# Performance work log

Hardware: AMD Instinct MI355X
Metric: run time of the kernel (lower is better)

## Reference

```python
import jax, jax.numpy as jnp
import numpy as np

B, H, S, D = 2, 16, 2048, 64
MASK_NEG = 1e9


def setup_inputs() -> dict:
    key = jax.random.key(0)
    kq, kk, kv, km = jax.random.split(key, 4)
    Q = jax.random.normal(kq, (B, H, S, D), dtype=jnp.float32)
    K = jax.random.normal(kk, (B, H, S, D), dtype=jnp.float32)
    V = jax.random.normal(kv, (B, H, S, D), dtype=jnp.float32)
    # float 0/1 mask, broadcast over heads; 1 = masked-out position
    attn_mask = jax.random.randint(km, (B, 1, S, S), 0, 2).astype(jnp.float32)
    return {"Q": Q, "K": K, "V": V, "attn_mask": attn_mask}


def reference(Q, K, V, attn_mask):
    # scores: [B, H, S, S]
    attn_score = jnp.einsum('bhqd,bhkd->bhqk', Q, K)
    scale = jnp.sqrt(jnp.asarray(K.shape[-1], dtype=jnp.float32))
    attn_scale = attn_score / scale - MASK_NEG * attn_mask
    attn_prob = jax.nn.softmax(attn_scale, axis=-1)
    attn_out = jnp.einsum('bhqk,bhkd->bhqd', attn_prob, V)
    return attn_out
```

## Files before the change

### kernel.cpp

```cpp
#include <hip/hip_runtime.h>


#define S_LEN 2048
#define D_DIM 64
#define WPR   32
#define NIT   32

typedef __attribute__((ext_vector_type(8)))  short bf16x8;
typedef __attribute__((ext_vector_type(4)))  float f32x4;
typedef __attribute__((ext_vector_type(16))) float f32x16;
typedef unsigned uint2v __attribute__((ext_vector_type(2)));
typedef unsigned long long ull;

__device__ __forceinline__ f32x16 mfma32(bf16x8 a, bf16x8 b, f32x16 c) {
  return __builtin_amdgcn_mfma_f32_32x32x16_bf16(a, b, c, 0, 0, 0);
}
__device__ __forceinline__ f32x4 mfma16(bf16x8 a, bf16x8 b, f32x4 c) {
  return __builtin_amdgcn_mfma_f32_16x16x32_bf16(a, b, c, 0, 0, 0);
}
__device__ __forceinline__ unsigned short f2bf(float f) {
  unsigned u = __builtin_bit_cast(unsigned, f);
  unsigned r = u + 0x7FFFu + ((u >> 16) & 1u);
  return (unsigned short)(r >> 16);
}
__device__ __forceinline__ float bf2f(unsigned short s) {
  unsigned u = ((unsigned)s) << 16;
  return __builtin_bit_cast(float, u);
}
__device__ __forceinline__ unsigned packbf(float a, float b) {
  unsigned r;
  asm("v_cvt_pk_bf16_f32 %0, %1, %2" : "=v"(r) : "v"(a), "v"(b));
  return r;
}
__device__ __forceinline__ float fexp2(float x) {
#if __has_builtin(__builtin_amdgcn_exp2f)
  return __builtin_amdgcn_exp2f(x);
#else
  return exp2f(x);
#endif
}
__device__ __forceinline__ bool detect_bf16(const void* maskp) {
  const unsigned short* s = (const unsigned short*)maskp;
  unsigned short v = s[2 * (threadIdx.x & 63)];
  return __ballot(v == (unsigned short)0x3F80) != 0ull;
}
__device__ __forceinline__ int4 cvt_f8(const float* p) {
  float4 f0 = *(const float4*)p;
  float4 f1 = *(const float4*)(p + 4);
  int4 r;
  r.x = (int)packbf(f0.x, f0.y);
  r.y = (int)packbf(f0.z, f0.w);
  r.z = (int)packbf(f1.x, f1.y);
  r.w = (int)packbf(f1.z, f1.w);
  return r;
}
__device__ __forceinline__ void gl_lds16(const unsigned short* g, unsigned short* l) {
#if __has_builtin(__builtin_amdgcn_global_load_lds)
  __builtin_amdgcn_global_load_lds(
      (const __attribute__((address_space(1))) unsigned int*)g,
      (__attribute__((address_space(3))) unsigned int*)l, 16, 0, 0);
#else
  *(int4*)((char*)l + (threadIdx.x & 63) * 16) = *(const int4*)g;
#endif
}

#define C1 0.18033688011112042f
#define C2 1.4426950408889634e9f

#define SEG0 4096u
#define SEG1 2048u
#define SEG2 1024u
#define SEG3 2048u

__global__ __launch_bounds__(256) void prep_all(
    const void* __restrict__ M, const void* __restrict__ Kin,
    const void* __restrict__ Vin, const void* __restrict__ Qin,
    ull* __restrict__ bits, unsigned short* __restrict__ Kf,
    unsigned short* __restrict__ Vf, unsigned short* __restrict__ Qc) {
  __shared__ __align__(16) unsigned short T[64 * 72];
  __shared__ ull rowb[32];
  const bool isb = detect_bf16(M);
  const unsigned bx = blockIdx.x;
  const int tid = threadIdx.x;

  if (bx < SEG0) {
    const unsigned bb = bx >> 11, q32 = (bx >> 5) & 63u, w = bx & 31u;
    const int wv = tid >> 6, l = tid & 63;
    #pragma unroll
    for (int j = 0; j < 8; ++j) {
      int rl = j * 4 + wv;
      size_t midx = ((size_t)(bb * 2048u + q32 * 32u + rl)) * 2048u + w * 64u + l;
      bool on = isb ? (bf2f(((const unsigned short*)M)[midx]) > 0.5f)
                    : (((const float*)M)[midx] > 0.5f);
      ull bm = __ballot(on);
      if (l == 0) rowb[rl] = bm;
    }
    __syncthreads();
    if (wv == 0) {
      const ull wc = rowb[l & 31];
      const int hi2 = l >> 5;
      ull* basep = bits + (((size_t)(bb * 32 + w)) << 11) + (size_t)q32 * 32;
      #pragma unroll
      for (int sub = 0; sub < 2; ++sub) {
        #pragma unroll
        for (int r = 0; r < 16; ++r) {
          int pos = sub * 32 + (r & 3) + 8 * (r >> 2) + 4 * hi2;
          ull W = __ballot(((wc >> pos) & 1ull) != 0ull);
          if (l == 0) basep[sub * 16 + r] = W;
        }
      }
    }
  } else if (bx < SEG0 + SEG1) {
    if (isb) return;
    unsigned g = (bx - SEG0) * 256u + tid;
    unsigned lane = g & 63u, f = (g >> 6) & 7u, it = (g >> 9) & 31u, bh = g >> 14;
    unsigned t = f >> 2, dc = f & 3, hi = lane >> 5, l31 = lane & 31;
    size_t src = (size_t)bh * (S_LEN * D_DIM) +
                 (size_t)(it * 64 + t * 32 + l31) * D_DIM + dc * 16 + hi * 8;
    *(int4*)&Kf[(size_t)g * 8] = cvt_f8((const float*)Kin + src);
  } else if (bx < SEG0 + SEG1 + SEG2) {
    unsigned idx = bx - (SEG0 + SEG1);
    unsigned bh = idx >> 5, it = idx & 31u;
    {
      int k = tid >> 2, d0 = (tid & 3) * 16;
      size_t src = (size_t)bh * (S_LEN * D_DIM) + (size_t)(it * 64 + k) * D_DIM + d0;
      int4 a, c;
      if (isb) {
        const unsigned short* s = (const unsigned short*)Vin + src;
        a = *(const int4*)s; c = *(const int4*)(s + 8);
      } else {
        const float* s = (const float*)Vin + src;
        a = cvt_f8(s); c = cvt_f8(s + 8);
      }
      *(int4*)&T[k * 72 + d0] = a;
      *(int4*)&T[k * 72 + d0 + 8] = c;
    }
    __syncthreads();
    #pragma unroll
    for (int h = 0; h < 2; ++h) {
      int c = tid + h * 256;
      int lane = c & 63, f = c >> 6;
      int t = f >> 2, kc = (f >> 1) & 1, dt = f & 1;
      int hi = lane >> 5, l31 = lane & 31;
      unsigned short v[8];
      #pragma unroll
      for (int j = 0; j < 8; ++j)
        v[j] = T[(t * 32 + kc * 16 + hi * 8 + j) * 72 + dt * 32 + l31];
      *(int4*)&Vf[(((size_t)(bh * 32 + it)) * 8 + f) * 512 + lane * 8] = *(int4*)v;
    }
  } else {
    if (isb) return;
    size_t i0 = ((size_t)(bx - (SEG0 + SEG1 + SEG2)) * 256 + tid) * 8;
    unsigned short v[8];
    const float* f = (const float*)Qin + i0;
    #pragma unroll
    for (int j = 0; j < 4; ++j)
      *((unsigned*)v + j) = packbf(f[2 * j] * C1, f[2 * j + 1] * C1);
    *(int4*)&Qc[i0] = *(int4*)v;
  }
}

__global__ __launch_bounds__(256, 4) void attn_fast(
    const unsigned short* __restrict__ Qc, const void* __restrict__ Qraw,
    const unsigned short* __restrict__ Kf, const void* __restrict__ Kraw,
    const unsigned short* __restrict__ Vf, const ull* __restrict__ Wm,
    const void* __restrict__ maskp, void* __restrict__ Op) {
  __shared__ __align__(16) unsigned short Stg[2][2][8][512];

  const bool isb = detect_bf16(maskp);
  const int tid  = threadIdx.x;
  const int wave = tid >> 6;
  const int lane = tid & 63;
  const int hi   = lane >> 5;
  const int l31  = lane & 31;
  const int wvu  = __builtin_amdgcn_readfirstlane(wave);
  const int g    = wvu >> 1;
  const int rw   = wvu & 1;
  const int id   = blockIdx.x;
  const int slot = id >> 3;
  const int bh   = (id & 7) * 4 + (slot & 3);
  const int qb   = slot >> 2;
  const int qbase = qb * 64 + rw * 32;
  const int b    = bh >> 4;
  const size_t base = (size_t)bh * S_LEN * D_DIM;
  const int xidx = ((lane ^ 32) & 63) * 4;

  bf16x8 qf[4];
  if (isb) {
    #pragma unroll
    for (int dc = 0; dc < 4; ++dc) {
      bf16x8 q = *(const bf16x8*)((const unsigned short*)Qraw + base +
                    (size_t)(qbase + l31) * D_DIM + dc * 16 + hi * 8);
      #pragma unroll
      for (int j = 0; j < 8; ++j)
        q[j] = (short)f2bf(bf2f((unsigned short)q[j]) * C1);
      qf[dc] = q;
    }
  } else {
    #pragma unroll
    for (int dc = 0; dc < 4; ++dc)
      qf[dc] = *(const bf16x8*)&Qc[base + (size_t)(qbase + l31) * D_DIM + dc * 16 + hi * 8];
  }

  bf16x8 onesb;
  #pragma unroll
  for (int i = 0; i < 8; ++i) onesb[i] = (short)0x3F80;

  const unsigned short* Kw0;
  size_t kd;
  if (isb) {
    Kw0 = (const unsigned short*)Kraw + base + (size_t)l31 * D_DIM + (2 * rw) * 16 + hi * 8;
    kd = 16;
  } else {
    Kw0 = Kf + (size_t)bh * 131072 + (size_t)(2 * rw) * 512 + lane * 8;
    kd = 512;
  }
  const unsigned short* Vw = Vf + (size_t)bh * 131072 + (size_t)(2 * rw) * 512 + lane * 8;
  const int ks0 = g * 32;

  const ull* WmU = Wm + (((size_t)(b * 32)) << 11) + (size_t)(qb * 2 + rw) * 32;

  f32x16 acc_o[2];
  f32x16 acc_l;
  f32x16 zv;
  #pragma unroll
  for (int r = 0; r < 16; ++r) {
    acc_o[0][r] = 0.f; acc_o[1][r] = 0.f; acc_l[r] = 0.f; zv[r] = 0.f;
  }

  {
    const size_t so = (size_t)ks0 * 2048;
    gl_lds16(Kw0 + so,      &Stg[g][0][2 * rw][0]);
    gl_lds16(Kw0 + so + kd, &Stg[g][0][2 * rw + 1][0]);
    gl_lds16(Vw + so,       &Stg[g][0][4 + 2 * rw][0]);
    gl_lds16(Vw + so + 512, &Stg[g][0][4 + 2 * rw + 1][0]);
  }
  __syncthreads();

  #pragma unroll 2
  for (int f = 0; f < 32; ++f) {
    const int cur = f & 1;
    if (f < 31) {
      const size_t so = (size_t)(ks0 + f + 1) * 2048;
      gl_lds16(Kw0 + so,      &Stg[g][cur ^ 1][2 * rw][0]);
      gl_lds16(Kw0 + so + kd, &Stg[g][cur ^ 1][2 * rw + 1][0]);
      gl_lds16(Vw + so,       &Stg[g][cur ^ 1][4 + 2 * rw][0]);
      gl_lds16(Vw + so + 512, &Stg[g][cur ^ 1][4 + 2 * rw + 1][0]);
    }
    const int ks = ks0 + f;
    const ull* Wp = WmU + (((size_t)(ks >> 1)) << 11) + (size_t)(ks & 1) * 16;

    bf16x8 ka[4];
    #pragma unroll
    for (int dc = 0; dc < 4; ++dc)
      ka[dc] = *(const bf16x8*)&Stg[g][cur][dc][lane * 8];
    __builtin_amdgcn_s_setprio(1);
    f32x16 sc0 = mfma32(ka[0], qf[0], zv);
    f32x16 sc1 = mfma32(ka[2], qf[2], zv);
    sc0 = mfma32(ka[1], qf[1], sc0);
    sc1 = mfma32(ka[3], qf[3], sc1);
    __builtin_amdgcn_s_setprio(0);

    float p[16];
    #pragma unroll
    for (int r = 0; r < 16; ++r) {
      float e = fexp2(sc0[r] + sc1[r]);
      ull mr = Wp[r];
      asm("v_cndmask_b32 %0, %1, 0, %2" : "=v"(p[r]) : "v"(e), "s"(mr));
    }

    #pragma unroll
    for (int kc = 0; kc < 2; ++kc) {
      unsigned pk0 = packbf(p[8 * kc + 0], p[8 * kc + 1]);
      unsigned pk1 = packbf(p[8 * kc + 2], p[8 * kc + 3]);
      unsigned pk2 = packbf(p[8 * kc + 4], p[8 * kc + 5]);
      unsigned pk3 = packbf(p[8 * kc + 6], p[8 * kc + 7]);
      uint4 d;
#if __has_builtin(__builtin_amdgcn_permlane32_swap)
      uint2v s02 = __builtin_amdgcn_permlane32_swap(pk0, pk2, false, false);
      uint2v s13 = __builtin_amdgcn_permlane32_swap(pk1, pk3, false, false);
      d.x = s02[0]; d.z = s02[1];
      d.y = s13[0]; d.w = s13[1];
#else
      unsigned x0 = (unsigned)__builtin_amdgcn_ds_bpermute(xidx, (int)pk0);
      unsigned x1 = (unsigned)__builtin_amdgcn_ds_bpermute(xidx, (int)pk1);
      unsigned x2 = (unsigned)__builtin_amdgcn_ds_bpermute(xidx, (int)pk2);
      unsigned x3 = (unsigned)__builtin_amdgcn_ds_bpermute(xidx, (int)pk3);
      d.x = hi ? x2 : pk0;
      d.y = hi ? x3 : pk1;
      d.z = hi ? pk2 : x0;
      d.w = hi ? pk3 : x1;
#endif
      bf16x8 pf = __builtin_bit_cast(bf16x8, d);
      __builtin_amdgcn_s_setprio(1);
      #pragma unroll
      for (int dt = 0; dt < 2; ++dt) {
        bf16x8 vfr = *(const bf16x8*)&Stg[g][cur][4 + kc * 2 + dt][lane * 8];
        acc_o[dt] = mfma32(pf, vfr, acc_o[dt]);
      }
      acc_l = mfma32(pf, onesb, acc_l);
      __builtin_amdgcn_s_setprio(0);
    }

    __syncthreads();
  }

  float* Cb = (float*)Stg;
  if (g == 1) {
    #pragma unroll
    for (int r = 0; r < 16; ++r) {
      Cb[(rw * 48 + r) * 64 + lane]      = acc_o[0][r];
      Cb[(rw * 48 + 16 + r) * 64 + lane] = acc_o[1][r];
      Cb[(rw * 48 + 32 + r) * 64 + lane] = acc_l[r];
    }
  }
  __syncthreads();
  if (g == 0) {
    #pragma unroll
    for (int r = 0; r < 16; ++r) {
      float o0 = acc_o[0][r] + Cb[(rw * 48 + r) * 64 + lane];
      float o1 = acc_o[1][r] + Cb[(rw * 48 + 16 + r) * 64 + lane];
      float lv = acc_l[r]    + Cb[(rw * 48 + 32 + r) * 64 + lane];
      int m = (r & 3) + 8 * (r >> 2) + 4 * hi;
      float inv = 1.0f / lv;
      size_t idx = base + (size_t)(qbase + m) * D_DIM + l31;
      if (isb) {
        ((unsigned short*)Op)[idx]      = f2bf(o0 * inv);
        ((unsigned short*)Op)[idx + 32] = f2bf(o1 * inv);
      } else {
        ((float*)Op)[idx]      = o0 * inv;
        ((float*)Op)[idx + 32] = o1 * inv;
      }
    }
  }
}

__global__ __launch_bounds__(256, 2) void attn_fallback(
    const void* __restrict__ Qp, const void* __restrict__ Kp,
    const void* __restrict__ Vp, const void* __restrict__ maskp,
    void* __restrict__ Op) {
  __shared__ __align__(16) short QKlds[128 * 72];
  __shared__ __align__(16) short Vtlds[64 * 72];
  __shared__ __align__(16) short Plds2[128 * 72];

  const bool isb = detect_bf16(maskp);
  const int tid  = threadIdx.x;
  const int wave = tid >> 6;
  const int lane = tid & 63;
  const int l15  = lane & 15;
  const int quad = lane >> 4;
  const int q0   = blockIdx.x * 128;
  const int bh   = blockIdx.y;
  const int b    = bh >> 4;
  const size_t base = (size_t)bh * S_LEN * D_DIM;

  const short* Qs = (const short*)Qp; const float* Qf = (const float*)Qp;
  const short* Ks = (const short*)Kp; const float* Kf2 = (const float*)Kp;
  const short* Vs = (const short*)Vp; const float* Vf2 = (const float*)Vp;

  if (isb) {
    const short* Qg = Qs + base + (size_t)q0 * D_DIM;
    #pragma unroll
    for (int p = 0; p < 4; ++p) {
      int e = p * 2048 + tid * 8;
      *(int4*)&QKlds[(e >> 6) * 72 + (e & 63)] = *(const int4*)(Qg + e);
    }
  } else {
    const float* Qg = Qf + base + (size_t)q0 * D_DIM;
    #pragma unroll
    for (int p = 0; p < 4; ++p) {
      int e = p * 2048 + tid * 8;
      *(int4*)&QKlds[(e >> 6) * 72 + (e & 63)] = cvt_f8(Qg + e);
    }
  }
  __syncthreads();
  bf16x8 qf[2][2];
  #pragma unroll
  for (int mi = 0; mi < 2; ++mi)
    #pragma unroll
    for (int kt = 0; kt < 2; ++kt)
      qf[mi][kt] = *(const bf16x8*)&QKlds[(wave * 32 + mi * 16 + l15) * 72 + kt * 32 + quad * 8];
  __syncthreads();

  f32x4 acc_o[2][4];
  f32x4 acc_l[2];
  const f32x4 zero4 = {0.f, 0.f, 0.f, 0.f};
  #pragma unroll
  for (int mi = 0; mi < 2; ++mi) {
    acc_l[mi] = zero4;
    #pragma unroll
    for (int nt = 0; nt < 4; ++nt) acc_o[mi][nt] = zero4;
  }
  bf16x8 onesB;
  {
    short ov = (l15 == 0) ? (short)0x3F80 : (short)0;
    #pragma unroll
    for (int i = 0; i < 8; ++i) onesB[i] = ov;
  }

  for (int it = 0; it < NIT; ++it) {
    const int k0 = it * 64;
    if (isb) {
      const short* Kg = Ks + base + (size_t)k0 * D_DIM;
      #pragma unroll
      for (int p = 0; p < 2; ++p) {
        int e = p * 2048 + tid * 8;
        *(int4*)&QKlds[(e >> 6) * 72 + (e & 63)] = *(const int4*)(Kg + e);
      }
    } else {
      const float* Kg = Kf2 + base + (size_t)k0 * D_DIM;
      #pragma unroll
      for (int p = 0; p < 2; ++p) {
        int e = p * 2048 + tid * 8;
        *(int4*)&QKlds[(e >> 6) * 72 + (e & 63)] = cvt_f8(Kg + e);
      }
    }
    {
      const int r0 = (tid >> 3) * 2;
      const int d0 = (tid & 7) * 8;
      unsigned short as_[8], bs_[8];
      if (isb) {
        const short* Vg = Vs + base + (size_t)k0 * D_DIM;
        *(int4*)as_ = *(const int4*)(Vg + r0 * D_DIM + d0);
        *(int4*)bs_ = *(const int4*)(Vg + (r0 + 1) * D_DIM + d0);
      } else {
        const float* Vg = Vf2 + base + (size_t)k0 * D_DIM;
        *(int4*)as_ = cvt_f8(Vg + r0 * D_DIM + d0);
        *(int4*)bs_ = cvt_f8(Vg + (r0 + 1) * D_DIM + d0);
      }
      #pragma unroll
      for (int j = 0; j < 8; ++j) {
        int d = d0 + j;
        int blk = (r0 >> 3) ^ (d >> 3);
        unsigned pk = (unsigned)as_[j] | ((unsigned)bs_[j] << 16);
        *(unsigned*)&Vtlds[d * 72 + blk * 8 + (r0 & 7)] = pk;
      }
    }
    __syncthreads();

    f32x4 sc[2][4];
    #pragma unroll
    for (int mi = 0; mi < 2; ++mi)
      #pragma unroll
      for (int nt = 0; nt < 4; ++nt) sc[mi][nt] = zero4;
    #pragma unroll
    for (int nt = 0; nt < 4; ++nt) {
      bf16x8 kf0 = *(const bf16x8*)&QKlds[(nt * 16 + l15) * 72 + quad * 8];
      bf16x8 kf1 = *(const bf16x8*)&QKlds[(nt * 16 + l15) * 72 + 32 + quad * 8];
      #pragma unroll
      for (int mi = 0; mi < 2; ++mi) {
        sc[mi][nt] = mfma16(qf[mi][0], kf0, sc[mi][nt]);
        sc[mi][nt] = mfma16(qf[mi][1], kf1, sc[mi][nt]);
      }
    }

    #pragma unroll
    for (int mi = 0; mi < 2; ++mi) {
      #pragma unroll
      for (int nt = 0; nt < 4; ++nt) {
        #pragma unroll
        for (int reg = 0; reg < 4; ++reg) {
          int rg = q0 + wave * 32 + mi * 16 + quad * 4 + reg;
          size_t mix = (size_t)b * S_LEN * S_LEN + (size_t)rg * S_LEN + k0 + nt * 16 + l15;
          float mv = isb ? bf2f(((const unsigned short*)maskp)[mix])
                         : ((const float*)maskp)[mix];
          float y = sc[mi][nt][reg] * C1 - mv * C2;
          Plds2[(wave * 32 + mi * 16 + quad * 4 + reg) * 72 + nt * 16 + l15] =
              (short)f2bf(fexp2(y));
        }
      }
    }
    __syncthreads();

    #pragma unroll
    for (int kt = 0; kt < 2; ++kt) {
      bf16x8 pf[2];
      #pragma unroll
      for (int mi = 0; mi < 2; ++mi)
        pf[mi] = *(const bf16x8*)&Plds2[(wave * 32 + mi * 16 + l15) * 72 + kt * 32 + quad * 8];
      #pragma unroll
      for (int nt = 0; nt < 4; ++nt) {
        int d = nt * 16 + l15;
        int kb = (kt * 4 + quad) ^ (d >> 3);
        bf16x8 vf = *(const bf16x8*)&Vtlds[d * 72 + kb * 8];
        #pragma unroll
        for (int mi = 0; mi < 2; ++mi)
          acc_o[mi][nt] = mfma16(pf[mi], vf, acc_o[mi][nt]);
      }
      #pragma unroll
      for (int mi = 0; mi < 2; ++mi)
        acc_l[mi] = mfma16(pf[mi], onesB, acc_l[mi]);
    }
    __syncthreads();
  }

  #pragma unroll
  for (int mi = 0; mi < 2; ++mi) {
    #pragma unroll
    for (int reg = 0; reg < 4; ++reg) {
      float lv = __shfl(acc_l[mi][reg], lane & 48, 64);
      float inv = 1.0f / lv;
      #pragma unroll
      for (int nt = 0; nt < 4; ++nt) {
        float o = acc_o[mi][nt][reg] * inv;
        size_t idx = base + (size_t)(q0 + wave * 32 + mi * 16 + quad * 4 + reg) * D_DIM + nt * 16 + l15;
        if (isb) ((unsigned short*)Op)[idx] = f2bf(o);
        else     ((float*)Op)[idx] = o;
      }
    }
  }
}

extern "C" void kernel_launch(void* const* d_in, const int* in_sizes, int n_in,
                              void* d_out, int out_size, void* d_ws, size_t ws_size,
                              hipStream_t stream) {
  const void* Q = d_in[0];
  const void* K = d_in[1];
  const void* V = d_in[2];
  const void* M = d_in[3];

  dim3 block(256);
  const size_t bits_bytes = (size_t)2 * S_LEN * S_LEN / 8;
  const size_t tens_bytes = (size_t)2 * 16 * S_LEN * D_DIM * 2;

  if (ws_size >= bits_bytes + 3 * tens_bytes) {
    char* ws = (char*)d_ws;
    ull* bits = (ull*)ws;
    unsigned short* Kf = (unsigned short*)(ws + bits_bytes);
    unsigned short* Vf = (unsigned short*)(ws + bits_bytes + tens_bytes);
    unsigned short* Qc = (unsigned short*)(ws + bits_bytes + 2 * tens_bytes);
    prep_all<<<dim3(SEG0 + SEG1 + SEG2 + SEG3), block, 0, stream>>>(
        M, K, V, Q, bits, Kf, Vf, Qc);
    attn_fast<<<dim3(1024), block, 0, stream>>>(Qc, Q, Kf, K, Vf, bits, M, d_out);
  } else {
    attn_fallback<<<dim3(S_LEN / 128, 32), block, 0, stream>>>(Q, K, V, M, d_out);
  }
}
```

Before: 168.4 us.

## Process two query tiles per wave to reuse staged K/V and drop ones-MFMA

Each wave now handles 64 query rows (two 32-row sub-tiles) against each staged K/V chunk, so K/V global loads and LDS reads are amortized over twice the queries and the grid is halved to 512 blocks. The row-sum is no longer computed with an extra MFMA against a ones vector. Instead it is accumulated in VALU from the fp32 probabilities, combined across lane halves with a bpermute, and reduced across waves through a small LDS array. The cost is higher register pressure (launch bounds lowered to 2 blocks/SM) and fewer blocks, which reduces occupancy and load balance across CUs.

```diff
diff --git a/kernel.cpp b/kernel.cpp
--- a/kernel.cpp
+++ b/kernel.cpp
@@ -160,12 +160,13 @@
   }
 }
 
-__global__ __launch_bounds__(256, 4) void attn_fast(
+__global__ __launch_bounds__(256, 2) void attn_fast(
     const unsigned short* __restrict__ Qc, const void* __restrict__ Qraw,
     const unsigned short* __restrict__ Kf, const void* __restrict__ Kraw,
     const unsigned short* __restrict__ Vf, const ull* __restrict__ Wm,
     const void* __restrict__ maskp, void* __restrict__ Op) {
   __shared__ __align__(16) unsigned short Stg[2][2][8][512];
+  __shared__ float Ls[4][2][32];
 
   const bool isb = detect_bf16(maskp);
   const int tid  = threadIdx.x;
@@ -180,31 +181,32 @@
   const int slot = id >> 3;
   const int bh   = (id & 7) * 4 + (slot & 3);
   const int qb   = slot >> 2;
-  const int qbase = qb * 64 + rw * 32;
+  const int qbase = qb * 128 + rw * 64;
   const int b    = bh >> 4;
   const size_t base = (size_t)bh * S_LEN * D_DIM;
   const int xidx = ((lane ^ 32) & 63) * 4;
 
-  bf16x8 qf[4];
+  bf16x8 qf[2][4];
   if (isb) {
     #pragma unroll
-    for (int dc = 0; dc < 4; ++dc) {
-      bf16x8 q = *(const bf16x8*)((const unsigned short*)Qraw + base +
-                    (size_t)(qbase + l31) * D_DIM + dc * 16 + hi * 8);
-      #pragma unroll
-      for (int j = 0; j < 8; ++j)
-        q[j] = (short)f2bf(bf2f((unsigned short)q[j]) * C1);
-      qf[dc] = q;
-    }
+    for (int u = 0; u < 2; ++u)
+      #pragma unroll
+      for (int dc = 0; dc < 4; ++dc) {
+        bf16x8 q = *(const bf16x8*)((const unsigned short*)Qraw + base +
+                      (size_t)(qbase + u * 32 + l31) * D_DIM + dc * 16 + hi * 8);
+        #pragma unroll
+        for (int j = 0; j < 8; ++j)
+          q[j] = (short)f2bf(bf2f((unsigned short)q[j]) * C1);
+        qf[u][dc] = q;
+      }
   } else {
     #pragma unroll
-    for (int dc = 0; dc < 4; ++dc)
-      qf[dc] = *(const bf16x8*)&Qc[base + (size_t)(qbase + l31) * D_DIM + dc * 16 + hi * 8];
-  }
-
-  bf16x8 onesb;
-  #pragma unroll
-  for (int i = 0; i < 8; ++i) onesb[i] = (short)0x3F80;
+    for (int u = 0; u < 2; ++u)
+      #pragma unroll
+      for (int dc = 0; dc < 4; ++dc)
+        qf[u][dc] = *(const bf16x8*)&Qc[base +
+                      (size_t)(qbase + u * 32 + l31) * D_DIM + dc * 16 + hi * 8];
+  }
 
   const unsigned short* Kw0;
   size_t kd;
@@ -218,15 +220,21 @@
   const unsigned short* Vw = Vf + (size_t)bh * 131072 + (size_t)(2 * rw) * 512 + lane * 8;
   const int ks0 = g * 32;
 
-  const ull* WmU = Wm + (((size_t)(b * 32)) << 11) + (size_t)(qb * 2 + rw) * 32;
-
-  f32x16 acc_o[2];
-  f32x16 acc_l;
+  const ull* WmU0 = Wm + (((size_t)(b * 32)) << 11) + (size_t)(qb * 4 + rw * 2) * 32;
+
+  f32x16 acc_o[2][2];
   f32x16 zv;
+  float ls[2][4];
   #pragma unroll
   for (int r = 0; r < 16; ++r) {
-    acc_o[0][r] = 0.f; acc_o[1][r] = 0.f; acc_l[r] = 0.f; zv[r] = 0.f;
-  }
+    acc_o[0][0][r] = 0.f; acc_o[0][1][r] = 0.f;
+    acc_o[1][0][r] = 0.f; acc_o[1][1][r] = 0.f;
+    zv[r] = 0.f;
+  }
+  #pragma unroll
+  for (int u = 0; u < 2; ++u)
+    #pragma unroll
+    for (int j = 0; j < 4; ++j) ls[u][j] = 0.f;
 
   {
     const size_t so = (size_t)ks0 * 2048;
@@ -248,90 +256,109 @@
       gl_lds16(Vw + so + 512, &Stg[g][cur ^ 1][4 + 2 * rw + 1][0]);
     }
     const int ks = ks0 + f;
-    const ull* Wp = WmU + (((size_t)(ks >> 1)) << 11) + (size_t)(ks & 1) * 16;
-
-    bf16x8 ka[4];
-    #pragma unroll
-    for (int dc = 0; dc < 4; ++dc)
-      ka[dc] = *(const bf16x8*)&Stg[g][cur][dc][lane * 8];
-    __builtin_amdgcn_s_setprio(1);
-    f32x16 sc0 = mfma32(ka[0], qf[0], zv);
-    f32x16 sc1 = mfma32(ka[2], qf[2], zv);
-    sc0 = mfma32(ka[1], qf[1], sc0);
-    sc1 = mfma32(ka[3], qf[3], sc1);
-    __builtin_amdgcn_s_setprio(0);
-
-    float p[16];
-    #pragma unroll
-    for (int r = 0; r < 16; ++r) {
-      float e = fexp2(sc0[r] + sc1[r]);
-      ull mr = Wp[r];
-      asm("v_cndmask_b32 %0, %1, 0, %2" : "=v"(p[r]) : "v"(e), "s"(mr));
-    }
-
-    #pragma unroll
-    for (int kc = 0; kc < 2; ++kc) {
-      unsigned pk0 = packbf(p[8 * kc + 0], p[8 * kc + 1]);
-      unsigned pk1 = packbf(p[8 * kc + 2], p[8 * kc + 3]);
-      unsigned pk2 = packbf(p[8 * kc + 4], p[8 * kc + 5]);
-      unsigned pk3 = packbf(p[8 * kc + 6], p[8 * kc + 7]);
-      uint4 d;
+    const ull* Wp0 = WmU0 + (((size_t)(ks >> 1)) << 11) + (size_t)(ks & 1) * 16;
+
+    bf16x8 ka[4], vf4[4];
+    #pragma unroll
+    for (int dc = 0; dc < 4; ++dc) {
+      ka[dc]  = *(const bf16x8*)&Stg[g][cur][dc][lane * 8];
+      vf4[dc] = *(const bf16x8*)&Stg[g][cur][4 + dc][lane * 8];
+    }
+
+    #pragma unroll
+    for (int u = 0; u < 2; ++u) {
+      const ull* Wp = Wp0 + u * 32;
+      __builtin_amdgcn_s_setprio(1);
+      f32x16 s0 = mfma32(ka[0], qf[u][0], zv);
+      f32x16 s1 = mfma32(ka[2], qf[u][2], zv);
+      s0 = mfma32(ka[1], qf[u][1], s0);
+      s1 = mfma32(ka[3], qf[u][3], s1);
+      __builtin_amdgcn_s_setprio(0);
+
+      float p[16];
+      #pragma unroll
+      for (int r = 0; r < 16; ++r) {
+        float e = fexp2(s0[r] + s1[r]);
+        ull mr = Wp[r];
+        asm("v_cndmask_b32 %0, %1, 0, %2" : "=v"(p[r]) : "v"(e), "s"(mr));
+      }
+      ls[u][0] += p[0] + p[4] + p[8]  + p[12];
+      ls[u][1] += p[1] + p[5] + p[9]  + p[13];
+      ls[u][2] += p[2] + p[6] + p[10] + p[14];
+      ls[u][3] += p[3] + p[7] + p[11] + p[15];
+
+      #pragma unroll
+      for (int kc = 0; kc < 2; ++kc) {
+        unsigned pk0 = packbf(p[8 * kc + 0], p[8 * kc + 1]);
+        unsigned pk1 = packbf(p[8 * kc + 2], p[8 * kc + 3]);
+        unsigned pk2 = packbf(p[8 * kc + 4], p[8 * kc + 5]);
+        unsigned pk3 = packbf(p[8 * kc + 6], p[8 * kc + 7]);
+        uint4 d;
 #if __has_builtin(__builtin_amdgcn_permlane32_swap)
-      uint2v s02 = __builtin_amdgcn_permlane32_swap(pk0, pk2, false, false);
-      uint2v s13 = __builtin_amdgcn_permlane32_swap(pk1, pk3, false, false);
-      d.x = s02[0]; d.z = s02[1];
-      d.y = s13[0]; d.w = s13[1];
+        uint2v s02 = __builtin_amdgcn_permlane32_swap(pk0, pk2, false, false);
+        uint2v s13 = __builtin_amdgcn_permlane32_swap(pk1, pk3, false, false);
+        d.x = s02[0]; d.z = s02[1];
+        d.y = s13[0]; d.w = s13[1];
 #else
-      unsigned x0 = (unsigned)__builtin_amdgcn_ds_bpermute(xidx, (int)pk0);
-      unsigned x1 = (unsigned)__builtin_amdgcn_ds_bpermute(xidx, (int)pk1);
-      unsigned x2 = (unsigned)__builtin_amdgcn_ds_bpermute(xidx, (int)pk2);
-      unsigned x3 = (unsigned)__builtin_amdgcn_ds_bpermute(xidx, (int)pk3);
-      d.x = hi ? x2 : pk0;
-      d.y = hi ? x3 : pk1;
-      d.z = hi ? pk2 : x0;
-      d.w = hi ? pk3 : x1;
+        unsigned x0 = (unsigned)__builtin_amdgcn_ds_bpermute(xidx, (int)pk0);
+        unsigned x1 = (unsigned)__builtin_amdgcn_ds_bpermute(xidx, (int)pk1);
+        unsigned x2 = (unsigned)__builtin_amdgcn_ds_bpermute(xidx, (int)pk2);
+        unsigned x3 = (unsigned)__builtin_amdgcn_ds_bpermute(xidx, (int)pk3);
+        d.x = hi ? x2 : pk0;
+        d.y = hi ? x3 : pk1;
+        d.z = hi ? pk2 : x0;
+        d.w = hi ? pk3 : x1;
 #endif
-      bf16x8 pf = __builtin_bit_cast(bf16x8, d);
-      __builtin_amdgcn_s_setprio(1);
-      #pragma unroll
-      for (int dt = 0; dt < 2; ++dt) {
-        bf16x8 vfr = *(const bf16x8*)&Stg[g][cur][4 + kc * 2 + dt][lane * 8];
-        acc_o[dt] = mfma32(pf, vfr, acc_o[dt]);
-      }
-      acc_l = mfma32(pf, onesb, acc_l);
-      __builtin_amdgcn_s_setprio(0);
+        bf16x8 pf = __builtin_bit_cast(bf16x8, d);
+        __builtin_amdgcn_s_setprio(1);
+        acc_o[u][0] = mfma32(pf, vf4[kc * 2 + 0], acc_o[u][0]);
+        acc_o[u][1] = mfma32(pf, vf4[kc * 2 + 1], acc_o[u][1]);
+        __builtin_amdgcn_s_setprio(0);
+      }
     }
 
     __syncthreads();
+  }
+
+  #pragma unroll
+  for (int u = 0; u < 2; ++u) {
+    float lsum = (ls[u][0] + ls[u][1]) + (ls[u][2] + ls[u][3]);
+    int li = __builtin_bit_cast(int, lsum);
+    float other = __builtin_bit_cast(float, __builtin_amdgcn_ds_bpermute(xidx, li));
+    lsum += other;
+    if (hi == 0) Ls[wave][u][l31] = lsum;
   }
 
   float* Cb = (float*)Stg;
   if (g == 1) {
     #pragma unroll
-    for (int r = 0; r < 16; ++r) {
-      Cb[(rw * 48 + r) * 64 + lane]      = acc_o[0][r];
-      Cb[(rw * 48 + 16 + r) * 64 + lane] = acc_o[1][r];
-      Cb[(rw * 48 + 32 + r) * 64 + lane] = acc_l[r];
-    }
+    for (int u = 0; u < 2; ++u)
+      #pragma unroll
+      for (int dt = 0; dt < 2; ++dt)
+        #pragma unroll
+        for (int r = 0; r < 16; ++r)
+          Cb[((size_t)(rw * 64 + u * 32 + dt * 16 + r)) * 64 + lane] = acc_o[u][dt][r];
   }
   __syncthreads();
   if (g == 0) {
     #pragma unroll
-    for (int r = 0; r < 16; ++r) {
-      float o0 = acc_o[0][r] + Cb[(rw * 48 + r) * 64 + lane];
-      float o1 = acc_o[1][r] + Cb[(rw * 48 + 16 + r) * 64 + lane];
-      float lv = acc_l[r]    + Cb[(rw * 48 + 32 + r) * 64 + lane];
-      int m = (r & 3) + 8 * (r >> 2) + 4 * hi;
-      float inv = 1.0f / lv;
-      size_t idx = base + (size_t)(qbase + m) * D_DIM + l31;
-      if (isb) {
-        ((unsigned short*)Op)[idx]      = f2bf(o0 * inv);
-        ((unsigned short*)Op)[idx + 32] = f2bf(o1 * inv);
-      } else {
-        ((float*)Op)[idx]      = o0 * inv;
-        ((float*)Op)[idx + 32] = o1 * inv;
-      }
-    }
+    for (int u = 0; u < 2; ++u)
+      #pragma unroll
+      for (int r = 0; r < 16; ++r) {
+        int m = (r & 3) + 8 * (r >> 2) + 4 * hi;
+        float lv = Ls[wave][u][m] + Ls[wave + 2][u][m];
+        float inv = 1.0f / lv;
+        float o0 = acc_o[u][0][r] + Cb[((size_t)(rw * 64 + u * 32 + r)) * 64 + lane];
+        float o1 = acc_o[u][1][r] + Cb[((size_t)(rw * 64 + u * 32 + 16 + r)) * 64 + lane];
+        size_t idx = base + (size_t)(qbase + u * 32 + m) * D_DIM + l31;
+        if (isb) {
+          ((unsigned short*)Op)[idx]      = f2bf(o0 * inv);
+          ((unsigned short*)Op)[idx + 32] = f2bf(o1 * inv);
+        } else {
+          ((float*)Op)[idx]      = o0 * inv;
+          ((float*)Op)[idx + 32] = o1 * inv;
+        }
+      }
   }
 }
 
@@ -531,7 +558,7 @@
     unsigned short* Qc = (unsigned short*)(ws + bits_bytes + 2 * tens_bytes);
     prep_all<<<dim3(SEG0 + SEG1 + SEG2 + SEG3), block, 0, stream>>>(
         M, K, V, Q, bits, Kf, Vf, Qc);
-    attn_fast<<<dim3(1024), block, 0, stream>>>(Qc, Q, Kf, K, Vf, bits, M, d_out);
+    attn_fast<<<dim3(512), block, 0, stream>>>(Qc, Q, Kf, K, Vf, bits, M, d_out);
   } else {
     attn_fallback<<<dim3(S_LEN / 128, 32), block, 0, stream>>>(Q, K, V, M, d_out);
   }
```

New measurement: 186.3 us. +10.6%, slower.
